# Kernel tuning notes

Hardware: AMD Instinct MI355X
Metric: run time of the kernel (lower is better)

Reference implementation:

```python
import jax, jax.numpy as jnp
from jax import lax
import numpy as np

K = 48          # dim_embedding_key
PAST = 20
FUT = 40
N = 65536       # total surrounding-agent nodes
E = 1048576     # edges
B = 1           # batch (structurally forced to 1 by the original code)


def conv1d_relu(x, w, b):
    # x: [B, 2, T], w: [K, 2, 3], padding=1 -> relu(Conv1d)
    y = lax.conv_general_dilated(x, w, (1,), ((1, 1),),
                                 dimension_numbers=('NCH', 'OIH', 'NCH'))
    return jax.nn.relu(y + b[None, :, None])


def gru_cell(xt, h, Wih, Whh, bih, bhh):
    gi = xt @ Wih.T + bih
    gh = h @ Whh.T + bhh
    ir, iz, inn = jnp.split(gi, 3, axis=-1)
    hr, hz, hn = jnp.split(gh, 3, axis=-1)
    r = jax.nn.sigmoid(ir + hr)
    z = jax.nn.sigmoid(iz + hz)
    n = jnp.tanh(inn + r * hn)
    return (1 - z) * n + z * h


def gru_last(x, Wih, Whh, bih, bhh):
    # x: [Nb, T, Din]; returns final hidden state [Nb, H] (torch GRU, h0 = 0)
    h0 = jnp.zeros((x.shape[0], Whh.shape[1]), x.dtype)
    def step(h, xt):
        h2 = gru_cell(xt, h, Wih, Whh, bih, bhh)
        return h2, None
    hT, _ = lax.scan(step, h0, jnp.swapaxes(x, 0, 1))
    return hT


def gcn_conv(x, row, col, w, W, b, n):
    # PyG GCNConv(normalize=True): add self loops (weight 1), symmetric norm,
    # x @ W.T, gather at source `row`, scatter-add at target `col`, + bias.
    loop = jnp.arange(n)
    row = jnp.concatenate([row, loop])
    col = jnp.concatenate([col, loop])
    w = jnp.concatenate([w, jnp.ones((n,), w.dtype)])
    deg = jax.ops.segment_sum(w, col, num_segments=n)
    dinv = jnp.where(deg > 0, lax.rsqrt(jnp.where(deg > 0, deg, 1.0)), 0.0)
    norm = dinv[row] * w * dinv[col]
    xw = x @ W.T
    msg = xw[row] * norm[:, None]
    return jax.ops.segment_sum(msg, col, num_segments=n) + b


def forward(past, future, x, edge_index, edge_weight,
            conv_past_w, conv_past_b, conv_fut_w, conv_fut_b,
            enc_past_Wih, enc_past_Whh, enc_past_bih, enc_past_bhh,
            enc_fut_Wih, enc_fut_Whh, enc_fut_bih, enc_fut_bhh,
            dec_Wih, dec_Whh, dec_bih, dec_bhh,
            fc_w, fc_b, gcn1_w, gcn1_b, gcn2_w, gcn2_b):
    present0 = past[:, -1, :2]                                  # [B, 2]

    # --- surrounding agents: conv1d + GRU encoder over all N nodes ---
    inter_past = jnp.swapaxes(x.reshape(-1, PAST, 2), 1, 2)     # [N, 2, T]
    story_embed = jnp.swapaxes(conv1d_relu(inter_past, conv_past_w, conv_past_b), 1, 2)
    state_past = gru_last(story_embed, enc_past_Wih, enc_past_Whh, enc_past_bih, enc_past_bhh)  # [N, K]

    # --- GCN interaction (edge_weight nonempty branch); dropout is eval-mode identity ---
    ei = edge_index.reshape(2, -1)
    ew = edge_weight.reshape(-1)
    x1 = jax.nn.relu(gcn_conv(state_past, ei[0], ei[1], ew, gcn1_w, gcn1_b, N))
    x1 = gcn_conv(x1, ei[0], ei[1], ew, gcn2_w, gcn2_b, N)
    interact_past = x1[0].reshape(B, -1)                        # [B, K] (B == 1)

    # --- ego past / future encoders ---
    past_embed = jnp.swapaxes(conv1d_relu(jnp.swapaxes(past, 1, 2), conv_past_w, conv_past_b), 1, 2)
    fut_embed = jnp.swapaxes(conv1d_relu(jnp.swapaxes(future, 1, 2), conv_fut_w, conv_fut_b), 1, 2)
    target_past = gru_last(past_embed, enc_past_Wih, enc_past_Whh, enc_past_bih, enc_past_bhh)   # [B, K]
    state_fut = gru_last(fut_embed, enc_fut_Wih, enc_fut_Whh, enc_fut_bih, enc_fut_bhh)          # [B, K]

    state_conc = jnp.concatenate([interact_past, target_past, state_fut], axis=-1)               # [B, 3K]

    zeros_in = jnp.zeros_like(state_conc)
    def step(carry, i):
        h, present = carry
        inp = jnp.where(i == 0, state_conc, zeros_in)
        h = gru_cell(inp, h, dec_Wih, dec_Whh, dec_bih, dec_bhh)
        coords = present + h @ fc_w.T + fc_b
        return (h, coords), coords
    (_, _), coords_seq = lax.scan(step, (jnp.zeros((B, 3 * K), past.dtype), present0), jnp.arange(FUT))
    return jnp.swapaxes(coords_seq, 0, 1)                        # [B, FUT, 2]


def setup_inputs() -> dict:
    ks = jax.random.split(jax.random.key(0), 32)
    def p(k, shape, s=0.1):
        return jax.random.normal(k, shape, jnp.float32) * s
    inp = {
        'past': p(ks[0], (B, PAST, 2), 1.0),
        'future': p(ks[1], (B, FUT, 2), 1.0),
        'x': p(ks[2], (N, PAST, 2), 1.0),
        'edge_index': jax.random.randint(ks[3], (1, 2, E), 0, N, jnp.int32),
        'edge_weight': jax.random.uniform(ks[4], (1, E), jnp.float32),
        'conv_past_w': p(ks[5], (K, 2, 3)), 'conv_past_b': p(ks[6], (K,)),
        'conv_fut_w': p(ks[7], (K, 2, 3)), 'conv_fut_b': p(ks[8], (K,)),
        'enc_past_Wih': p(ks[9], (3 * K, K)), 'enc_past_Whh': p(ks[10], (3 * K, K)),
        'enc_past_bih': p(ks[11], (3 * K,)), 'enc_past_bhh': p(ks[12], (3 * K,)),
        'enc_fut_Wih': p(ks[13], (3 * K, K)), 'enc_fut_Whh': p(ks[14], (3 * K, K)),
        'enc_fut_bih': p(ks[15], (3 * K,)), 'enc_fut_bhh': p(ks[16], (3 * K,)),
        'dec_Wih': p(ks[17], (9 * K, 3 * K)), 'dec_Whh': p(ks[18], (9 * K, 3 * K)),
        'dec_bih': p(ks[19], (9 * K,)), 'dec_bhh': p(ks[20], (9 * K,)),
        'fc_w': p(ks[21], (2, 3 * K)), 'fc_b': p(ks[22], (2,)),
        'gcn1_w': p(ks[23], (K, K)), 'gcn1_b': p(ks[24], (K,)),
        'gcn2_w': p(ks[25], (K, K)), 'gcn2_b': p(ks[26], (K,)),
    }
    return inp


def reference(past, future, x, edge_index, edge_weight,
              conv_past_w, conv_past_b, conv_fut_w, conv_fut_b,
              enc_past_Wih, enc_past_Whh, enc_past_bih, enc_past_bhh,
              enc_fut_Wih, enc_fut_Whh, enc_fut_bih, enc_fut_bhh,
              dec_Wih, dec_Whh, dec_bih, dec_bhh,
              fc_w, fc_b, gcn1_w, gcn1_b, gcn2_w, gcn2_b):
    return forward(past, future, x, edge_index, edge_weight,
                   conv_past_w, conv_past_b, conv_fut_w, conv_fut_b,
                   enc_past_Wih, enc_past_Whh, enc_past_bih, enc_past_bhh,
                   enc_fut_Wih, enc_fut_Whh, enc_fut_bih, enc_fut_bhh,
                   dec_Wih, dec_Whh, dec_bih, dec_bhh,
                   fc_w, fc_b, gcn1_w, gcn1_b, gcn2_w, gcn2_b)
```

## Files before the change

### kernel.cpp

```cpp
#include <hip/hip_runtime.h>
#include <math.h>

#define NN 65536
#define NE 1048576
#define KH 48
#define G3 144
#define DEGB 512

#define CAP_L1 8192
#define CAP_S1 4096
#define CAP_E2 65536
#define CAP_S2 8192

#define OFF_MARK1  0u
#define OFF_MARK2  262144u
#define OFF_CNT    524288u
#define OFF_L1R    524352u
#define OFF_L1W    557120u
#define OFF_S1G    589888u
#define OFF_E2R    606272u
#define OFF_E2S    868416u
#define OFF_E2W    1130560u
#define OFF_S2     1392704u
#define OFF_DEG2   1425472u
#define OFF_STATE  1458240u
#define OFF_X1     3031104u
#define OFF_TPSF   3817536u

typedef _Float16 h2_t __attribute__((ext_vector_type(2)));

__device__ __forceinline__ float sigmf(float x) { return 1.0f / (1.0f + expf(-x)); }

#if __has_builtin(__builtin_amdgcn_fdot2)
__device__ __forceinline__ float fdot2f(h2_t a, h2_t b, float c) {
    return __builtin_amdgcn_fdot2(a, b, c, false);
}
#else
__device__ __forceinline__ float fdot2f(h2_t a, h2_t b, float c) {
    return c + (float)a.x * (float)b.x + (float)a.y * (float)b.y;
}
#endif

__global__ void k_edges1(const int* ei, const float* ew,
                         int* mark1, unsigned* cnt, int* l1r, float* l1w) {
    int q = blockIdx.x * blockDim.x + threadIdx.x;
    if (q >= NE / 4) return;
    if (q == 0) mark1[0] = 1;
    int4 c4 = reinterpret_cast<const int4*>(ei + NE)[q];
    int e = q * 4;
    int cc[4] = {c4.x, c4.y, c4.z, c4.w};
#pragma unroll
    for (int j = 0; j < 4; ++j) {
        if (cc[j] == 0) {
            int r = ei[e + j];
            float w = ew[e + j];
            unsigned s = atomicAdd(&cnt[0], 1u);
            if (s < CAP_L1) { l1r[s] = r; l1w[s] = w; }
            mark1[r] = 1;
        }
    }
}

__global__ void k_compact1(int* mark1, int* mark2, unsigned* cnt,
                           int* e2r, int* e2s, float* e2w, int* s1g,
                           float* x1, const float* g1b) {
    int i = blockIdx.x * blockDim.x + threadIdx.x;
    if (i >= NN) return;
    if (mark1[i]) {
        unsigned s = atomicAdd(&cnt[1], 1u);
        if (s < CAP_S1) {
            mark1[i] = (int)s + 1;
            mark2[i] = 1;
            s1g[s] = i;
            unsigned t = atomicAdd(&cnt[2], 1u);
            if (t < CAP_E2) { e2r[t] = i; e2s[t] = (int)s; e2w[t] = 1.0f; }
            for (int k = 0; k < KH; ++k) x1[s * KH + k] = g1b[k];
        } else {
            mark1[i] = 0;
        }
    }
}

__global__ void k_edges2(const int* ei, const float* ew,
                         const int* mark1, int* mark2, unsigned* cnt,
                         int* e2r, int* e2s, float* e2w) {
    int q = blockIdx.x * blockDim.x + threadIdx.x;
    if (q >= NE / 4) return;
    int4 c4 = reinterpret_cast<const int4*>(ei + NE)[q];
    int e = q * 4;
    int cc[4] = {c4.x, c4.y, c4.z, c4.w};
#pragma unroll
    for (int j = 0; j < 4; ++j) {
        int m = mark1[cc[j]];
        if (m > 0) {
            int r = ei[e + j];
            float w = ew[e + j];
            unsigned s = atomicAdd(&cnt[2], 1u);
            if (s < CAP_E2) { e2r[s] = r; e2s[s] = m - 1; e2w[s] = w; }
            mark2[r] = 1;
        }
    }
}

__global__ void k_compact2(int* mark2, unsigned* cnt, int* s2, float* deg2) {
    int i = blockIdx.x * blockDim.x + threadIdx.x;
    if (i >= NN) return;
    if (mark2[i]) {
        unsigned s = atomicAdd(&cnt[3], 1u);
        if (s < CAP_S2) { s2[s] = i; mark2[i] = (int)s + 1; deg2[s] = 1.0f; }
        else mark2[i] = 0;
    }
}

__device__ void gru_seq(const float* xseq, int T,
                        const float* cw, const float* cb,
                        const float* Wih, const float* Whh,
                        const float* bih, const float* bhh,
                        float* out48,
                        float* s_x, float* s_embed, float* s_giA,
                        float* s_h, float* s_gh) {
    int t = threadIdx.x;
    int nt = blockDim.x;
    for (int i = t; i < T * 2; i += nt) s_x[i] = xseq[i];
    __syncthreads();
    for (int idx = t; idx < T * KH; idx += nt) {
        int tt = idx / KH;
        int k = idx - tt * KH;
        float acc = cb[k];
#pragma unroll
        for (int d = 0; d < 3; ++d) {
            int tau = tt + d - 1;
            if (tau >= 0 && tau < T) {
                acc += cw[k * 6 + d] * s_x[tau * 2 + 0];
                acc += cw[k * 6 + 3 + d] * s_x[tau * 2 + 1];
            }
        }
        s_embed[tt * KH + k] = fmaxf(acc, 0.0f);
    }
    __syncthreads();
    for (int idx = t; idx < T * G3; idx += nt) {
        int step = idx / G3;
        int row = idx - step * G3;
        const float4* wp = reinterpret_cast<const float4*>(Wih + row * KH);
        const float4* em = reinterpret_cast<const float4*>(s_embed + step * KH);
        float g = bih[row];
#pragma unroll
        for (int j = 0; j < 12; ++j) {
            float4 w4 = wp[j]; float4 e4 = em[j];
            g += w4.x * e4.x + w4.y * e4.y + w4.z * e4.z + w4.w * e4.w;
        }
        s_giA[idx] = g;
    }
    float4 wh[12];
    float bh = 0.0f;
    if (t < G3) {
        const float4* q = reinterpret_cast<const float4*>(Whh + t * KH);
#pragma unroll
        for (int j = 0; j < 12; ++j) wh[j] = q[j];
        bh = bhh[t];
    }
    if (t < KH) s_h[t] = 0.0f;
    __syncthreads();
    for (int step = 0; step < T; ++step) {
        if (t < G3) {
            const float4* hp = reinterpret_cast<const float4*>(s_h);
            float g = bh;
#pragma unroll
            for (int j = 0; j < 12; ++j) {
                float4 h4 = hp[j];
                g += wh[j].x * h4.x + wh[j].y * h4.y + wh[j].z * h4.z + wh[j].w * h4.w;
            }
            s_gh[t] = g;
        }
        __syncthreads();
        if (t < KH) {
            const float* gi = s_giA + step * G3;
            float r = sigmf(gi[t] + s_gh[t]);
            float z = sigmf(gi[KH + t] + s_gh[KH + t]);
            float n = tanhf(gi[2 * KH + t] + r * s_gh[2 * KH + t]);
            s_h[t] = (1.0f - z) * n + z * s_h[t];
        }
        __syncthreads();
    }
    if (t < KH) out48[t] = s_h[t];
}

__global__ __launch_bounds__(192, 2) void k_gru(
    const float* x, const float* cpw, const float* cpb,
    const float* epWih, const float* epWhh, const float* epbih, const float* epbhh,
    const float* cfw, const float* cfb,
    const float* efWih, const float* efWhh, const float* efbih, const float* efbhh,
    const float* past, const float* future,
    const int* ei, const float* ew, const int* mark2, float* deg2,
    const int* s2, const unsigned* cnt, float* state, float* tpsf) {
    if (blockIdx.x < DEGB) {
        int per = NE / DEGB;
        int lo = blockIdx.x * per;
        for (int e = lo + threadIdx.x; e < lo + per; e += blockDim.x) {
            int c = ei[NE + e];
            int m = mark2[c];
            if (m > 0) atomicAdd(&deg2[m - 1], ew[e]);
        }
        return;
    }
    __shared__ __align__(16) float s_x[80];
    __shared__ __align__(16) float s_embed[40 * KH];
    __shared__ __align__(16) float s_giA[40 * G3];
    __shared__ __align__(16) float s_h[KH];
    __shared__ float s_gh[G3];
    if (blockIdx.x == DEGB) {
        gru_seq(past, 20, cpw, cpb, epWih, epWhh, epbih, epbhh,
                tpsf, s_x, s_embed, s_giA, s_h, s_gh);
        return;
    }
    if (blockIdx.x == DEGB + 1) {
        gru_seq(future, 40, cfw, cfb, efWih, efWhh, efbih, efbhh,
                tpsf + 64, s_x, s_embed, s_giA, s_h, s_gh);
        return;
    }
    int b0 = blockIdx.x - (DEGB + 2);
    int nw = gridDim.x - (DEGB + 2);
    int cnt2 = (int)min(cnt[3], (unsigned)CAP_S2);
    for (int b = b0; b < cnt2; b += nw) {
        int node = s2[b];
        gru_seq(x + (size_t)node * 40, 20, cpw, cpb, epWih, epWhh, epbih, epbhh,
                state + (size_t)b * KH, s_x, s_embed, s_giA, s_h, s_gh);
    }
}

__global__ void k_acc1(const unsigned* cnt, const int* e2r, const int* e2s,
                       const float* e2w, const int* mark2, const float* deg2,
                       const int* s1g, const float* state,
                       const float* W1, float* x1) {
    int nE = (int)min(cnt[2], (unsigned)CAP_E2);
    int total = nE * KH;
    int stride = gridDim.x * blockDim.x;
    for (int idx = blockIdx.x * blockDim.x + threadIdx.x; idx < total; idx += stride) {
        int e = idx / KH;
        int k = idx - e * KH;
        int row = e2r[e];
        int s2i = mark2[row] - 1;
        if (s2i < 0) continue;
        int cglob = s1g[e2s[e]];
        int cs2 = mark2[cglob] - 1;
        float norm = e2w[e] * rsqrtf(deg2[s2i] * deg2[cs2]);
        const float* sp = state + (size_t)s2i * KH;
        const float* wp = W1 + k * KH;
        float acc = 0.0f;
#pragma unroll
        for (int m = 0; m < KH; ++m) acc += sp[m] * wp[m];
        atomicAdd(&x1[e2s[e] * KH + k], acc * norm);
    }
}

__global__ __launch_bounds__(896, 4) void k_dec(
    const unsigned* cnt, const int* l1r, const float* l1w,
    const int* mark1, const int* mark2, const float* deg2, const float* x1,
    const float* W2, const float* b2, const float* tpsf, const float* past,
    const float* dWih, const float* dWhh, const float* dbih, const float* dbhh,
    const float* fcw, const float* fcb, float* out) {
    __shared__ __align__(16) float s_conc[G3];
    __shared__ __align__(16) float s_h[G3];
    __shared__ __align__(8) _Float16 s_h16[G3];
    __shared__ float s_gi0[3 * G3], s_gh[3 * G3], s_bih[3 * G3];
    int t = threadIdx.x;
    if (t < 48) s_conc[t] = b2[t];
    else if (t < 96) s_conc[t] = tpsf[t - 48];
    else if (t < 144) s_conc[t] = tpsf[64 + t - 96];
    if (t < 3 * G3) s_bih[t] = dbih[t];
    if (t < G3) { s_h[t] = 0.0f; s_h16[t] = (_Float16)0.0f; }
    __syncthreads();
    int cl1 = (int)min(cnt[0], (unsigned)CAP_L1);
    float dinv0 = rsqrtf(deg2[mark2[0] - 1]);
    int items = (cl1 + 1) * KH;
    for (int idx = t; idx < items; idx += blockDim.x) {
        int e = idx / KH;
        int k = idx - e * KH;
        int row; float norm;
        if (e == cl1) { row = 0; norm = dinv0 * dinv0; }
        else {
            row = l1r[e];
            int rs2 = mark2[row] - 1;
            if (rs2 < 0) continue;
            norm = l1w[e] * rsqrtf(deg2[rs2]) * dinv0;
        }
        int s1 = mark1[row] - 1;
        if (s1 < 0) continue;
        const float* xp = x1 + (size_t)s1 * KH;
        const float* wp = W2 + k * KH;
        float acc = 0.0f;
#pragma unroll
        for (int m = 0; m < KH; ++m) acc += fmaxf(xp[m], 0.0f) * wp[m];
        atomicAdd(&s_conc[k], acc * norm);
    }
    int row = t >> 1, hf = t & 1;
    h2_t wh[36];
    float bh2 = 0.0f;
    if (t < 864) {
        const float4* q = reinterpret_cast<const float4*>(dWhh + row * G3 + hf * 72);
#pragma unroll
        for (int jj = 0; jj < 18; ++jj) {
            float4 f = q[jj];
            h2_t a, b;
            a.x = (_Float16)f.x; a.y = (_Float16)f.y;
            b.x = (_Float16)f.z; b.y = (_Float16)f.w;
            wh[2 * jj] = a; wh[2 * jj + 1] = b;
        }
        if (hf == 0) bh2 = dbhh[row];
    }
    float pres = 0.0f;
    if (t == 0 || t == 64) pres = past[38 + (t >> 6)];
    __syncthreads();
    if (t < 864) {
        const float4* p = reinterpret_cast<const float4*>(dWih + row * G3 + hf * 72);
        const float4* cc = reinterpret_cast<const float4*>(s_conc + hf * 72);
        float g = 0.0f;
#pragma unroll
        for (int j = 0; j < 18; ++j) {
            float4 w4 = p[j]; float4 c4 = cc[j];
            g += w4.x * c4.x + w4.y * c4.y + w4.z * c4.z + w4.w * c4.w;
        }
        g += __shfl_xor(g, 1);
        if (hf == 0) s_gi0[row] = g + s_bih[row];
    }
    for (int i = 0; i < 40; ++i) {
        if (t < 864) {
            const h2_t* hp = reinterpret_cast<const h2_t*>(s_h16 + hf * 72);
            float g = 0.0f;
#pragma unroll
            for (int j = 0; j < 36; ++j) g = fdot2f(wh[j], hp[j], g);
            g += __shfl_xor(g, 1);
            if (hf == 0) s_gh[row] = g + bh2;
        }
        __syncthreads();
        if (t < G3) {
            float gr = (i == 0) ? s_gi0[t] : s_bih[t];
            float gz = (i == 0) ? s_gi0[G3 + t] : s_bih[G3 + t];
            float gn = (i == 0) ? s_gi0[2 * G3 + t] : s_bih[2 * G3 + t];
            float r = sigmf(gr + s_gh[t]);
            float z = sigmf(gz + s_gh[G3 + t]);
            float n = tanhf(gn + r * s_gh[2 * G3 + t]);
            float hnew = (1.0f - z) * n + z * s_h[t];
            s_h[t] = hnew;
            s_h16[t] = (_Float16)hnew;
        }
        __syncthreads();
        int w = t >> 6;
        if (w < 2) {
            int lane = t & 63;
            float p = 0.0f;
            for (int m = lane; m < G3; m += 64) p += s_h[m] * fcw[w * G3 + m];
#pragma unroll
            for (int off = 32; off > 0; off >>= 1) p += __shfl_down(p, off);
            if (lane == 0) {
                pres += p + fcb[w];
                out[i * 2 + w] = pres;
            }
        }
    }
}

extern "C" void kernel_launch(void* const* d_in, const int* in_sizes, int n_in,
                              void* d_out, int out_size, void* d_ws, size_t ws_size,
                              hipStream_t stream) {
    (void)in_sizes; (void)n_in; (void)out_size; (void)ws_size;
    const float* past   = (const float*)d_in[0];
    const float* future = (const float*)d_in[1];
    const float* x      = (const float*)d_in[2];
    const int*   ei     = (const int*)d_in[3];
    const float* ew     = (const float*)d_in[4];
    const float* cpw    = (const float*)d_in[5];
    const float* cpb    = (const float*)d_in[6];
    const float* cfw    = (const float*)d_in[7];
    const float* cfb    = (const float*)d_in[8];
    const float* epWih  = (const float*)d_in[9];
    const float* epWhh  = (const float*)d_in[10];
    const float* epbih  = (const float*)d_in[11];
    const float* epbhh  = (const float*)d_in[12];
    const float* efWih  = (const float*)d_in[13];
    const float* efWhh  = (const float*)d_in[14];
    const float* efbih  = (const float*)d_in[15];
    const float* efbhh  = (const float*)d_in[16];
    const float* dWih   = (const float*)d_in[17];
    const float* dWhh   = (const float*)d_in[18];
    const float* dbih   = (const float*)d_in[19];
    const float* dbhh   = (const float*)d_in[20];
    const float* fcw    = (const float*)d_in[21];
    const float* fcb    = (const float*)d_in[22];
    const float* g1w    = (const float*)d_in[23];
    const float* g1b    = (const float*)d_in[24];
    const float* g2w    = (const float*)d_in[25];
    const float* g2b    = (const float*)d_in[26];

    char* ws = (char*)d_ws;
    int*      mark1 = (int*)(ws + OFF_MARK1);
    int*      mark2 = (int*)(ws + OFF_MARK2);
    unsigned* cnt   = (unsigned*)(ws + OFF_CNT);
    int*      l1r   = (int*)(ws + OFF_L1R);
    float*    l1w   = (float*)(ws + OFF_L1W);
    int*      s1g   = (int*)(ws + OFF_S1G);
    int*      e2r   = (int*)(ws + OFF_E2R);
    int*      e2s   = (int*)(ws + OFF_E2S);
    float*    e2w   = (float*)(ws + OFF_E2W);
    int*      s2    = (int*)(ws + OFF_S2);
    float*    deg2  = (float*)(ws + OFF_DEG2);
    float*    state = (float*)(ws + OFF_STATE);
    float*    x1    = (float*)(ws + OFF_X1);
    float*    tpsf  = (float*)(ws + OFF_TPSF);

    hipMemsetAsync(ws, 0, 524352, stream);
    k_edges1<<<NE / 4 / 256, 256, 0, stream>>>(ei, ew, mark1, cnt, l1r, l1w);
    k_compact1<<<NN / 256, 256, 0, stream>>>(mark1, mark2, cnt, e2r, e2s, e2w, s1g, x1, g1b);
    k_edges2<<<NE / 4 / 256, 256, 0, stream>>>(ei, ew, mark1, mark2, cnt, e2r, e2s, e2w);
    k_compact2<<<NN / 256, 256, 0, stream>>>(mark2, cnt, s2, deg2);
    k_gru<<<DEGB + 2 + 512, 192, 0, stream>>>(x, cpw, cpb, epWih, epWhh, epbih, epbhh,
                                              cfw, cfb, efWih, efWhh, efbih, efbhh,
                                              past, future, ei, ew, mark2, deg2,
                                              s2, cnt, state, tpsf);
    k_acc1<<<128, 256, 0, stream>>>(cnt, e2r, e2s, e2w, mark2, deg2, s1g, state, g1w, x1);
    k_dec<<<1, 896, 0, stream>>>(cnt, l1r, l1w, mark1, mark2, deg2, x1, g2w, g2b,
                                 tpsf, past, dWih, dWhh, dbih, dbhh, fcw, fcb,
                                 (float*)d_out);
}
```

Measured before the change: 256.3 us.

## Fuse graph preprocessing, GRU and GCN stages into one cooperative kernel

Replaces the memset and six separate launches with one cooperative persistent kernel of 256 blocks that uses grid-wide syncs between the edge marking, compaction, degree, GRU, and GCN aggregation phases. The decoder moves to a separate 448-thread kernel in which each thread computes a full gate row, which removes the shuffle-based half-row reduction. This targets launch overhead and idle gaps between kernels. The costs are far fewer blocks for the edge-scan and GRU phases, serialized grid barriers, and the degree accumulation no longer overlapping the GRU work.

```diff
diff --git a/kernel.cpp b/kernel.cpp
--- a/kernel.cpp
+++ b/kernel.cpp
@@ -1,11 +1,14 @@
 #include <hip/hip_runtime.h>
+#include <hip/hip_cooperative_groups.h>
 #include <math.h>
+
+namespace cg = cooperative_groups;
 
 #define NN 65536
 #define NE 1048576
 #define KH 48
 #define G3 144
-#define DEGB 512
+#define GRID 256
 
 #define CAP_L1 8192
 #define CAP_S1 4096
@@ -26,8 +29,10 @@
 #define OFF_STATE  1458240u
 #define OFF_X1     3031104u
 #define OFF_TPSF   3817536u
+#define OFF_CONC   3818048u
 
 typedef _Float16 h2_t __attribute__((ext_vector_type(2)));
+struct __align__(16) h2x4 { h2_t a, b, c, d; };
 
 __device__ __forceinline__ float sigmf(float x) { return 1.0f / (1.0f + expf(-x)); }
 
@@ -40,77 +45,6 @@
     return c + (float)a.x * (float)b.x + (float)a.y * (float)b.y;
 }
 #endif
-
-__global__ void k_edges1(const int* ei, const float* ew,
-                         int* mark1, unsigned* cnt, int* l1r, float* l1w) {
-    int q = blockIdx.x * blockDim.x + threadIdx.x;
-    if (q >= NE / 4) return;
-    if (q == 0) mark1[0] = 1;
-    int4 c4 = reinterpret_cast<const int4*>(ei + NE)[q];
-    int e = q * 4;
-    int cc[4] = {c4.x, c4.y, c4.z, c4.w};
-#pragma unroll
-    for (int j = 0; j < 4; ++j) {
-        if (cc[j] == 0) {
-            int r = ei[e + j];
-            float w = ew[e + j];
-            unsigned s = atomicAdd(&cnt[0], 1u);
-            if (s < CAP_L1) { l1r[s] = r; l1w[s] = w; }
-            mark1[r] = 1;
-        }
-    }
-}
-
-__global__ void k_compact1(int* mark1, int* mark2, unsigned* cnt,
-                           int* e2r, int* e2s, float* e2w, int* s1g,
-                           float* x1, const float* g1b) {
-    int i = blockIdx.x * blockDim.x + threadIdx.x;
-    if (i >= NN) return;
-    if (mark1[i]) {
-        unsigned s = atomicAdd(&cnt[1], 1u);
-        if (s < CAP_S1) {
-            mark1[i] = (int)s + 1;
-            mark2[i] = 1;
-            s1g[s] = i;
-            unsigned t = atomicAdd(&cnt[2], 1u);
-            if (t < CAP_E2) { e2r[t] = i; e2s[t] = (int)s; e2w[t] = 1.0f; }
-            for (int k = 0; k < KH; ++k) x1[s * KH + k] = g1b[k];
-        } else {
-            mark1[i] = 0;
-        }
-    }
-}
-
-__global__ void k_edges2(const int* ei, const float* ew,
-                         const int* mark1, int* mark2, unsigned* cnt,
-                         int* e2r, int* e2s, float* e2w) {
-    int q = blockIdx.x * blockDim.x + threadIdx.x;
-    if (q >= NE / 4) return;
-    int4 c4 = reinterpret_cast<const int4*>(ei + NE)[q];
-    int e = q * 4;
-    int cc[4] = {c4.x, c4.y, c4.z, c4.w};
-#pragma unroll
-    for (int j = 0; j < 4; ++j) {
-        int m = mark1[cc[j]];
-        if (m > 0) {
-            int r = ei[e + j];
-            float w = ew[e + j];
-            unsigned s = atomicAdd(&cnt[2], 1u);
-            if (s < CAP_E2) { e2r[s] = r; e2s[s] = m - 1; e2w[s] = w; }
-            mark2[r] = 1;
-        }
-    }
-}
-
-__global__ void k_compact2(int* mark2, unsigned* cnt, int* s2, float* deg2) {
-    int i = blockIdx.x * blockDim.x + threadIdx.x;
-    if (i >= NN) return;
-    if (mark2[i]) {
-        unsigned s = atomicAdd(&cnt[3], 1u);
-        if (s < CAP_S2) { s2[s] = i; mark2[i] = (int)s + 1; deg2[s] = 1.0f; }
-        else mark2[i] = 0;
-    }
-}
 
 __device__ void gru_seq(const float* xseq, int T,
                         const float* cw, const float* cb,
@@ -185,57 +119,114 @@
     if (t < KH) out48[t] = s_h[t];
 }
 
-__global__ __launch_bounds__(192, 2) void k_gru(
-    const float* x, const float* cpw, const float* cpb,
+__global__ __launch_bounds__(256, 2) void k_all(
+    const float* past, const float* future, const float* x,
+    const int* ei, const float* ew,
+    const float* cpw, const float* cpb, const float* cfw, const float* cfb,
     const float* epWih, const float* epWhh, const float* epbih, const float* epbhh,
-    const float* cfw, const float* cfb,
     const float* efWih, const float* efWhh, const float* efbih, const float* efbhh,
-    const float* past, const float* future,
-    const int* ei, const float* ew, const int* mark2, float* deg2,
-    const int* s2, const unsigned* cnt, float* state, float* tpsf) {
-    if (blockIdx.x < DEGB) {
-        int per = NE / DEGB;
-        int lo = blockIdx.x * per;
-        for (int e = lo + threadIdx.x; e < lo + per; e += blockDim.x) {
-            int c = ei[NE + e];
-            int m = mark2[c];
-            if (m > 0) atomicAdd(&deg2[m - 1], ew[e]);
-        }
-        return;
-    }
+    const float* g1w, const float* g1b, const float* g2w, const float* g2b,
+    int* mark1, int* mark2, unsigned* cnt,
+    int* l1r, float* l1w, int* s1g,
+    int* e2r, int* e2s, float* e2w,
+    int* s2, float* deg2, float* state, float* x1, float* tpsf,
+    float* conc_g) {
     __shared__ __align__(16) float s_x[80];
     __shared__ __align__(16) float s_embed[40 * KH];
     __shared__ __align__(16) float s_giA[40 * G3];
-    __shared__ __align__(16) float s_h[KH];
-    __shared__ float s_gh[G3];
-    if (blockIdx.x == DEGB) {
-        gru_seq(past, 20, cpw, cpb, epWih, epWhh, epbih, epbhh,
-                tpsf, s_x, s_embed, s_giA, s_h, s_gh);
-        return;
-    }
-    if (blockIdx.x == DEGB + 1) {
-        gru_seq(future, 40, cfw, cfb, efWih, efWhh, efbih, efbhh,
-                tpsf + 64, s_x, s_embed, s_giA, s_h, s_gh);
-        return;
-    }
-    int b0 = blockIdx.x - (DEGB + 2);
-    int nw = gridDim.x - (DEGB + 2);
+    __shared__ __align__(16) float s_hG[KH];
+    __shared__ float s_ghG[G3];
+    __shared__ __align__(16) float s_conc[G3];
+
+    cg::grid_group grid = cg::this_grid();
+    int tid = blockIdx.x * blockDim.x + threadIdx.x;
+    int nth = gridDim.x * blockDim.x;
+
+    for (int i = tid; i < NN; i += nth) { mark1[i] = (i == 0) ? 1 : 0; mark2[i] = 0; }
+    if (tid < 16) cnt[tid] = 0;
+    grid.sync();
+
+    for (int q = tid; q < NE / 4; q += nth) {
+        int4 c4 = reinterpret_cast<const int4*>(ei + NE)[q];
+        int e = q * 4;
+        int cc[4] = {c4.x, c4.y, c4.z, c4.w};
+#pragma unroll
+        for (int j = 0; j < 4; ++j) {
+            if (cc[j] == 0) {
+                int r = ei[e + j];
+                float w = ew[e + j];
+                unsigned s = atomicAdd(&cnt[0], 1u);
+                if (s < CAP_L1) { l1r[s] = r; l1w[s] = w; }
+                mark1[r] = 1;
+            }
+        }
+    }
+    grid.sync();
+
+    for (int i = tid; i < NN; i += nth) {
+        if (mark1[i]) {
+            unsigned s = atomicAdd(&cnt[1], 1u);
+            if (s < CAP_S1) {
+                mark1[i] = (int)s + 1;
+                mark2[i] = 1;
+                s1g[s] = i;
+                unsigned t2 = atomicAdd(&cnt[2], 1u);
+                if (t2 < CAP_E2) { e2r[t2] = i; e2s[t2] = (int)s; e2w[t2] = 1.0f; }
+                for (int k = 0; k < KH; ++k) x1[s * KH + k] = g1b[k];
+            } else mark1[i] = 0;
+        }
+    }
+    grid.sync();
+
+    for (int q = tid; q < NE / 4; q += nth) {
+        int4 c4 = reinterpret_cast<const int4*>(ei + NE)[q];
+        int e = q * 4;
+        int cc[4] = {c4.x, c4.y, c4.z, c4.w};
+#pragma unroll
+        for (int j = 0; j < 4; ++j) {
+            int m = mark1[cc[j]];
+            if (m > 0) {
+                int r = ei[e + j];
+                float w = ew[e + j];
+                unsigned s = atomicAdd(&cnt[2], 1u);
+                if (s < CAP_E2) { e2r[s] = r; e2s[s] = m - 1; e2w[s] = w; }
+                mark2[r] = 1;
+            }
+        }
+    }
+    grid.sync();
+
+    for (int i = tid; i < NN; i += nth) {
+        if (mark2[i]) {
+            unsigned s = atomicAdd(&cnt[3], 1u);
+            if (s < CAP_S2) { s2[s] = i; mark2[i] = (int)s + 1; deg2[s] = 1.0f; }
+            else mark2[i] = 0;
+        }
+    }
+    grid.sync();
+
+    for (int e = tid; e < NE; e += nth) {
+        int c = ei[NE + e];
+        int m = mark2[c];
+        if (m > 0) atomicAdd(&deg2[m - 1], ew[e]);
+    }
     int cnt2 = (int)min(cnt[3], (unsigned)CAP_S2);
-    for (int b = b0; b < cnt2; b += nw) {
-        int node = s2[b];
-        gru_seq(x + (size_t)node * 40, 20, cpw, cpb, epWih, epWhh, epbih, epbhh,
-                state + (size_t)b * KH, s_x, s_embed, s_giA, s_h, s_gh);
-    }
-}
-
-__global__ void k_acc1(const unsigned* cnt, const int* e2r, const int* e2s,
-                       const float* e2w, const int* mark2, const float* deg2,
-                       const int* s1g, const float* state,
-                       const float* W1, float* x1) {
+    for (int it = blockIdx.x; it < cnt2 + 2; it += gridDim.x) {
+        if (it < cnt2) {
+            gru_seq(x + (size_t)s2[it] * 40, 20, cpw, cpb, epWih, epWhh, epbih, epbhh,
+                    state + (size_t)it * KH, s_x, s_embed, s_giA, s_hG, s_ghG);
+        } else if (it == cnt2) {
+            gru_seq(past, 20, cpw, cpb, epWih, epWhh, epbih, epbhh,
+                    tpsf, s_x, s_embed, s_giA, s_hG, s_ghG);
+        } else {
+            gru_seq(future, 40, cfw, cfb, efWih, efWhh, efbih, efbhh,
+                    tpsf + 64, s_x, s_embed, s_giA, s_hG, s_ghG);
+        }
+    }
+    grid.sync();
+
     int nE = (int)min(cnt[2], (unsigned)CAP_E2);
-    int total = nE * KH;
-    int stride = gridDim.x * blockDim.x;
-    for (int idx = blockIdx.x * blockDim.x + threadIdx.x; idx < total; idx += stride) {
+    for (int idx = tid; idx < nE * KH; idx += nth) {
         int e = idx / KH;
         int k = idx - e * KH;
         int row = e2r[e];
@@ -245,35 +236,24 @@
         int cs2 = mark2[cglob] - 1;
         float norm = e2w[e] * rsqrtf(deg2[s2i] * deg2[cs2]);
         const float* sp = state + (size_t)s2i * KH;
-        const float* wp = W1 + k * KH;
+        const float* wp = g1w + k * KH;
         float acc = 0.0f;
 #pragma unroll
         for (int m = 0; m < KH; ++m) acc += sp[m] * wp[m];
         atomicAdd(&x1[e2s[e] * KH + k], acc * norm);
     }
-}
-
-__global__ __launch_bounds__(896, 4) void k_dec(
-    const unsigned* cnt, const int* l1r, const float* l1w,
-    const int* mark1, const int* mark2, const float* deg2, const float* x1,
-    const float* W2, const float* b2, const float* tpsf, const float* past,
-    const float* dWih, const float* dWhh, const float* dbih, const float* dbhh,
-    const float* fcw, const float* fcb, float* out) {
-    __shared__ __align__(16) float s_conc[G3];
-    __shared__ __align__(16) float s_h[G3];
-    __shared__ __align__(8) _Float16 s_h16[G3];
-    __shared__ float s_gi0[3 * G3], s_gh[3 * G3], s_bih[3 * G3];
+    grid.sync();
+
+    if (blockIdx.x != 0) return;
     int t = threadIdx.x;
-    if (t < 48) s_conc[t] = b2[t];
+    if (t < 48) s_conc[t] = g2b[t];
     else if (t < 96) s_conc[t] = tpsf[t - 48];
     else if (t < 144) s_conc[t] = tpsf[64 + t - 96];
-    if (t < 3 * G3) s_bih[t] = dbih[t];
-    if (t < G3) { s_h[t] = 0.0f; s_h16[t] = (_Float16)0.0f; }
     __syncthreads();
     int cl1 = (int)min(cnt[0], (unsigned)CAP_L1);
     float dinv0 = rsqrtf(deg2[mark2[0] - 1]);
     int items = (cl1 + 1) * KH;
-    for (int idx = t; idx < items; idx += blockDim.x) {
+    for (int idx = t; idx < items; idx += 256) {
         int e = idx / KH;
         int k = idx - e * KH;
         int row; float norm;
@@ -287,50 +267,69 @@
         int s1 = mark1[row] - 1;
         if (s1 < 0) continue;
         const float* xp = x1 + (size_t)s1 * KH;
-        const float* wp = W2 + k * KH;
+        const float* wp = g2w + k * KH;
         float acc = 0.0f;
 #pragma unroll
         for (int m = 0; m < KH; ++m) acc += fmaxf(xp[m], 0.0f) * wp[m];
         atomicAdd(&s_conc[k], acc * norm);
     }
-    int row = t >> 1, hf = t & 1;
-    h2_t wh[36];
-    float bh2 = 0.0f;
-    if (t < 864) {
-        const float4* q = reinterpret_cast<const float4*>(dWhh + row * G3 + hf * 72);
-#pragma unroll
-        for (int jj = 0; jj < 18; ++jj) {
-            float4 f = q[jj];
-            h2_t a, b;
-            a.x = (_Float16)f.x; a.y = (_Float16)f.y;
-            b.x = (_Float16)f.z; b.y = (_Float16)f.w;
-            wh[2 * jj] = a; wh[2 * jj + 1] = b;
-        }
-        if (hf == 0) bh2 = dbhh[row];
+    __syncthreads();
+    if (t < G3) conc_g[t] = s_conc[t];
+}
+
+__global__ __launch_bounds__(448, 2) void k_dec2(
+    const float* conc_g, const float* past,
+    const float* dWih, const float* dWhh, const float* dbih, const float* dbhh,
+    const float* fcw, const float* fcb, float* out) {
+    __shared__ __align__(16) float s_conc[G3];
+    __shared__ __align__(16) float s_hD[G3];
+    __shared__ __align__(16) _Float16 s_h16[G3];
+    __shared__ float s_gi0[3 * G3], s_gh[3 * G3], s_bih[3 * G3];
+    int t = threadIdx.x;
+    if (t < G3) s_conc[t] = conc_g[t];
+    for (int i = t; i < 3 * G3; i += 448) s_bih[i] = dbih[i];
+    if (t < G3) { s_hD[t] = 0.0f; s_h16[t] = (_Float16)0.0f; }
+    h2x4 wr[18];
+    float bh = 0.0f;
+    if (t < 3 * G3) {
+        const float4* q = reinterpret_cast<const float4*>(dWhh + t * G3);
+#pragma unroll
+        for (int j = 0; j < 18; ++j) {
+            float4 a = q[2 * j], b = q[2 * j + 1];
+            wr[j].a = h2_t{(_Float16)a.x, (_Float16)a.y};
+            wr[j].b = h2_t{(_Float16)a.z, (_Float16)a.w};
+            wr[j].c = h2_t{(_Float16)b.x, (_Float16)b.y};
+            wr[j].d = h2_t{(_Float16)b.z, (_Float16)b.w};
+        }
+        bh = dbhh[t];
     }
     float pres = 0.0f;
     if (t == 0 || t == 64) pres = past[38 + (t >> 6)];
     __syncthreads();
-    if (t < 864) {
-        const float4* p = reinterpret_cast<const float4*>(dWih + row * G3 + hf * 72);
-        const float4* cc = reinterpret_cast<const float4*>(s_conc + hf * 72);
+    if (t < 3 * G3) {
+        const float4* p = reinterpret_cast<const float4*>(dWih + t * G3);
+        const float4* cc = reinterpret_cast<const float4*>(s_conc);
         float g = 0.0f;
 #pragma unroll
-        for (int j = 0; j < 18; ++j) {
+        for (int j = 0; j < 36; ++j) {
             float4 w4 = p[j]; float4 c4 = cc[j];
             g += w4.x * c4.x + w4.y * c4.y + w4.z * c4.z + w4.w * c4.w;
         }
-        g += __shfl_xor(g, 1);
-        if (hf == 0) s_gi0[row] = g + s_bih[row];
+        s_gi0[t] = g + s_bih[t];
     }
     for (int i = 0; i < 40; ++i) {
-        if (t < 864) {
-            const h2_t* hp = reinterpret_cast<const h2_t*>(s_h16 + hf * 72);
+        if (t < 3 * G3) {
+            const h2x4* hp = reinterpret_cast<const h2x4*>(s_h16);
             float g = 0.0f;
 #pragma unroll
-            for (int j = 0; j < 36; ++j) g = fdot2f(wh[j], hp[j], g);
-            g += __shfl_xor(g, 1);
-            if (hf == 0) s_gh[row] = g + bh2;
+            for (int j = 0; j < 18; ++j) {
+                h2x4 h = hp[j];
+                g = fdot2f(wr[j].a, h.a, g);
+                g = fdot2f(wr[j].b, h.b, g);
+                g = fdot2f(wr[j].c, h.c, g);
+                g = fdot2f(wr[j].d, h.d, g);
+            }
+            s_gh[t] = g + bh;
         }
         __syncthreads();
         if (t < G3) {
@@ -340,20 +339,20 @@
             float r = sigmf(gr + s_gh[t]);
             float z = sigmf(gz + s_gh[G3 + t]);
             float n = tanhf(gn + r * s_gh[2 * G3 + t]);
-            float hnew = (1.0f - z) * n + z * s_h[t];
-            s_h[t] = hnew;
+            float hnew = (1.0f - z) * n + z * s_hD[t];
+            s_hD[t] = hnew;
             s_h16[t] = (_Float16)hnew;
         }
         __syncthreads();
         int w = t >> 6;
         if (w < 2) {
             int lane = t & 63;
-            float p = 0.0f;
-            for (int m = lane; m < G3; m += 64) p += s_h[m] * fcw[w * G3 + m];
-#pragma unroll
-            for (int off = 32; off > 0; off >>= 1) p += __shfl_down(p, off);
+            float pp = 0.0f;
+            for (int m = lane; m < G3; m += 64) pp += s_hD[m] * fcw[w * G3 + m];
+#pragma unroll
+            for (int off = 32; off > 0; off >>= 1) pp += __shfl_down(pp, off);
             if (lane == 0) {
-                pres += p + fcb[w];
+                pres += pp + fcb[w];
                 out[i * 2 + w] = pres;
             }
         }
@@ -407,18 +406,21 @@
     float*    state = (float*)(ws + OFF_STATE);
     float*    x1    = (float*)(ws + OFF_X1);
     float*    tpsf  = (float*)(ws + OFF_TPSF);
-
-    hipMemsetAsync(ws, 0, 524352, stream);
-    k_edges1<<<NE / 4 / 256, 256, 0, stream>>>(ei, ew, mark1, cnt, l1r, l1w);
-    k_compact1<<<NN / 256, 256, 0, stream>>>(mark1, mark2, cnt, e2r, e2s, e2w, s1g, x1, g1b);
-    k_edges2<<<NE / 4 / 256, 256, 0, stream>>>(ei, ew, mark1, mark2, cnt, e2r, e2s, e2w);
-    k_compact2<<<NN / 256, 256, 0, stream>>>(mark2, cnt, s2, deg2);
-    k_gru<<<DEGB + 2 + 512, 192, 0, stream>>>(x, cpw, cpb, epWih, epWhh, epbih, epbhh,
-                                              cfw, cfb, efWih, efWhh, efbih, efbhh,
-                                              past, future, ei, ew, mark2, deg2,
-                                              s2, cnt, state, tpsf);
-    k_acc1<<<128, 256, 0, stream>>>(cnt, e2r, e2s, e2w, mark2, deg2, s1g, state, g1w, x1);
-    k_dec<<<1, 896, 0, stream>>>(cnt, l1r, l1w, mark1, mark2, deg2, x1, g2w, g2b,
-                                 tpsf, past, dWih, dWhh, dbih, dbhh, fcw, fcb,
-                                 (float*)d_out);
-}
+    float*    conc  = (float*)(ws + OFF_CONC);
+    float*    out   = (float*)d_out;
+
+    void* args[] = {
+        &past, &future, &x, &ei, &ew,
+        &cpw, &cpb, &cfw, &cfb,
+        &epWih, &epWhh, &epbih, &epbhh,
+        &efWih, &efWhh, &efbih, &efbhh,
+        &g1w, &g1b, &g2w, &g2b,
+        &mark1, &mark2, &cnt,
+        &l1r, &l1w, &s1g,
+        &e2r, &e2s, &e2w,
+        &s2, &deg2, &state, &x1, &tpsf,
+        &conc
+    };
+    hipLaunchCooperativeKernel((void*)k_all, dim3(GRID), dim3(256), args, 0, stream);
+    k_dec2<<<1, 448, 0, stream>>>(conc, past, dWih, dWhh, dbih, dbhh, fcw, fcb, out);
+}
```

New measurement: 454.1 us. 77.1% more time.
